# Optimization experiments

Hardware: AMD Instinct MI355X
Metric: run time of the kernel (lower is better)

## Reference

```python
import jax, jax.numpy as jnp
import numpy as np

SCALE = 8.0  # sqrt(d_k=64)


def setup_inputs() -> dict:
    key = jax.random.key(0)
    kq, kk, kv, km = jax.random.split(key, 4)
    B, L, D = 8, 4096, 64
    q = jax.random.normal(kq, (B, L, D), dtype=jnp.float32)
    k = jax.random.normal(kk, (B, L, D), dtype=jnp.float32)
    v = jax.random.normal(kv, (B, L, D), dtype=jnp.float32)
    mask = jax.random.randint(km, (B, L, L), 0, 2) == 1  # True = masked out
    return {"q": q, "k": k, "v": v, "mask": mask}


def reference(q, k, v, mask):
    # scores: [B, Lq, Lk]
    u = jnp.einsum('bqd,bkd->bqk', q, k) / SCALE
    u = jnp.where(mask, -jnp.inf, u)
    attn = jax.nn.softmax(u, axis=2)
    output = jnp.einsum('bqk,bkd->bqd', attn, v)
    return (attn, output)
```

## Files before the change

### kernel.cpp

```cpp
#include <hip/hip_runtime.h>
#include <hip/hip_bf16.h>
#include <stdint.h>

#define BB 8
#define LL 4096
#define DD 64
#define KT 64
#define NT (LL / KT)

typedef short bf16x8 __attribute__((ext_vector_type(8)));
typedef short bf16x4 __attribute__((ext_vector_type(4)));
typedef float f32x4 __attribute__((ext_vector_type(4)));

#define QSCALE 0.1803368801111204f
#define PP 68
#define MP 72

__device__ inline short f2bfs(float x) {
    __hip_bfloat16 h = __float2bfloat16(x);
    return __builtin_bit_cast(short, h);
}

__device__ inline int swzK(int r) { return (r & 3) | (((r >> 3) & 1) << 2); }
__device__ inline int swzV(int r) { return (r & 7) ^ ((r >> 3) & 7); }

__device__ inline void wg_barrier() {
    asm volatile("s_waitcnt lgkmcnt(0)" ::: "memory");
    __builtin_amdgcn_s_barrier();
    __builtin_amdgcn_sched_barrier(0);
}

__global__ void detect_mask_kernel(const uint32_t* __restrict__ w, uint32_t* __restrict__ flag) {
    __shared__ int nonbin;
    if (threadIdx.x == 0) nonbin = 0;
    __syncthreads();
    int bad = 0;
    for (int i = threadIdx.x; i < 4096; i += 256) bad |= (w[i] > 1u) ? 1 : 0;
    if (bad) atomicOr(&nonbin, 1);
    __syncthreads();
    if (threadIdx.x == 0) *flag = (uint32_t)(nonbin != 0);
}

__global__ __launch_bounds__(512, 4) void fused_attn_kernel(
    const float* __restrict__ qg, const float* __restrict__ kg,
    const float* __restrict__ vg, const void* __restrict__ maskv,
    const uint32_t* __restrict__ flagp,
    float* __restrict__ attn, float* __restrict__ outp)
{
    __shared__ alignas(16) ushort Kt[2][KT * 64];
    __shared__ alignas(16) ushort Vt[2][64 * KT];
    __shared__ alignas(16) float  Pout[64 * PP];
    __shared__ alignas(16) uint8_t Mt[2][64 * MP];
    __shared__ float Rs[128];

    const int tid = (int)threadIdx.x;
    const int w   = tid >> 6, l = tid & 63;
    const int lr  = l & 15, lg = l >> 4;
    const int rg  = w & 3, ch = w >> 2;
    const int id  = (int)blockIdx.x;
    const int b   = id & 7;
    const int q0  = (id >> 3) * 64;
    const bool mbyte = (*flagp != 0);

    const float* kb = kg + (size_t)b * LL * DD;
    const float* vb = vg + (size_t)b * LL * DD;
    const uint8_t* mb8 = (const uint8_t*)maskv + (size_t)b * LL * LL;
    float* attnb = attn + (size_t)b * LL * LL;
    const int qrow = q0 + 16 * rg + lr;
    const int* mrow32 = (const int*)maskv + (size_t)b * LL * LL + (size_t)qrow * LL + ch * 32 + lg * 8;

    bf16x8 qf0, qf1;
    {
        const float* qp = qg + (size_t)(b * LL + qrow) * DD + lg * 8;
        f32x4 a0 = *(const f32x4*)(qp)      * QSCALE, a1 = *(const f32x4*)(qp + 4)  * QSCALE;
        f32x4 a2 = *(const f32x4*)(qp + 32) * QSCALE, a3 = *(const f32x4*)(qp + 36) * QSCALE;
        #pragma unroll
        for (int e = 0; e < 4; ++e) { qf0[e] = f2bfs(a0[e]); qf0[4 + e] = f2bfs(a1[e]); }
        #pragma unroll
        for (int e = 0; e < 4; ++e) { qf1[e] = f2bfs(a2[e]); qf1[4 + e] = f2bfs(a3[e]); }
    }

    const int sr = tid >> 4, sc = tid & 15;
    const int mr = tid >> 3, mc = tid & 7;
    f32x4 kS0, kS1, vS0, vS1;
    uint64_t mS = 0;

    auto issK = [&](int kt) {
        const float* p = kb + (size_t)(kt * KT + sr) * DD + sc * 4;
        kS0 = *(const f32x4*)p;
        kS1 = *(const f32x4*)(p + 32 * DD);
    };
    auto issV = [&](int kt) {
        const float* p = vb + (size_t)(kt * KT + sr) * DD + sc * 4;
        vS0 = *(const f32x4*)p;
        vS1 = *(const f32x4*)(p + 32 * DD);
    };
    auto issM = [&](int kt) {
        if (mbyte) mS = *(const uint64_t*)(mb8 + (size_t)(q0 + mr) * LL + kt * KT + mc * 8);
    };
    auto comK = [&](int buf) {
        bf16x4 a, c;
        #pragma unroll
        for (int e = 0; e < 4; ++e) { a[e] = f2bfs(kS0[e]); c[e] = f2bfs(kS1[e]); }
        *(bf16x4*)&Kt[buf][sr * 64 + (((sc >> 1) ^ swzK(sr)) << 3) + (sc & 1) * 4] = a;
        const int r1 = sr + 32;
        *(bf16x4*)&Kt[buf][r1 * 64 + (((sc >> 1) ^ swzK(r1)) << 3) + (sc & 1) * 4] = c;
    };
    auto comV = [&](int buf) {
        #pragma unroll
        for (int e = 0; e < 4; ++e) {
            const int d = sc * 4 + e;
            Vt[buf][d * 64 + (((sr >> 3) ^ swzV(d)) << 3) + (sr & 7)]        = (ushort)f2bfs(vS0[e]);
            Vt[buf][d * 64 + ((((sr + 32) >> 3) ^ swzV(d)) << 3) + (sr & 7)] = (ushort)f2bfs(vS1[e]);
        }
    };
    auto comM = [&](int buf) {
        if (mbyte) *(uint64_t*)&Mt[buf][mr * MP + mc * 8] = mS;
    };

    float rsum = 0.f;
    f32x4 oacc[4];
    #pragma unroll
    for (int g = 0; g < 4; ++g) { f32x4 z = {0.f, 0.f, 0.f, 0.f}; oacc[g] = z; }

    auto body1 = [&](int cur, int kt) {
        uint64_t mu = 0;
        int4 mi0 = {0,0,0,0}, mi1 = {0,0,0,0};
        if (mbyte) mu = *(const uint64_t*)&Mt[cur][(16 * rg + lr) * MP + ch * 32 + lg * 8];
        else { mi0 = *(const int4*)(mrow32 + kt * KT); mi1 = *(const int4*)(mrow32 + kt * KT + 4); }
        float p8[8];
        #pragma unroll
        for (int n = 0; n < 2; ++n) {
            const int krow = ch * 32 + ((lr >> 2) << 3) + (n << 2) + (lr & 3);
            bf16x8 k0 = *(const bf16x8*)&Kt[cur][krow * 64 + ((lg       ^ swzK(krow)) << 3)];
            bf16x8 k1 = *(const bf16x8*)&Kt[cur][krow * 64 + (((4 + lg) ^ swzK(krow)) << 3)];
            f32x4 c = {0.f, 0.f, 0.f, 0.f};
            c = __builtin_amdgcn_mfma_f32_16x16x32_bf16(k0, qf0, c, 0, 0, 0);
            c = __builtin_amdgcn_mfma_f32_16x16x32_bf16(k1, qf1, c, 0, 0, 0);
            #pragma unroll
            for (int j = 0; j < 4; ++j) {
                const int t = n * 4 + j;
                int mk;
                if (mbyte) mk = (int)((mu >> (8 * t)) & 0xffu);
                else {
                    const int4 mi = n ? mi1 : mi0;
                    mk = (j == 0) ? mi.x : (j == 1) ? mi.y : (j == 2) ? mi.z : mi.w;
                }
                const float pv = mk ? 0.f : exp2f(c[j]);
                rsum += pv;
                p8[t] = pv;
            }
        }
        bf16x8 pa;
        #pragma unroll
        for (int t = 0; t < 8; ++t) pa[t] = f2bfs(p8[t]);
        __builtin_amdgcn_s_setprio(1);
        #pragma unroll
        for (int g = 0; g < 4; ++g) {
            const int d = g * 16 + lr;
            bf16x8 vf = *(const bf16x8*)&Vt[cur][d * 64 + (((ch * 4 + lg) ^ swzV(d)) << 3)];
            oacc[g] = __builtin_amdgcn_mfma_f32_16x16x32_bf16(pa, vf, oacc[g], 0, 0, 0);
        }
        __builtin_amdgcn_s_setprio(0);
    };

    issK(0); issV(0); issM(0);
    comK(0); comV(0); comM(0);
    wg_barrier();
    #pragma unroll 1
    for (int kt = 0; kt < NT; ++kt) {
        const int cur = kt & 1;
        const bool more = (kt < NT - 1);
        if (more) { issK(kt + 1); issV(kt + 1); issM(kt + 1); }
        body1(cur, kt);
        if (more) { comK(cur ^ 1); comV(cur ^ 1); comM(cur ^ 1); }
        wg_barrier();
    }

    rsum += __shfl_xor(rsum, 16, 64);
    rsum += __shfl_xor(rsum, 32, 64);
    if (lg == 0) Rs[ch * 64 + 16 * rg + lr] = rsum;
    __syncthreads();
    const float rinv = 1.0f / (Rs[16 * rg + lr] + Rs[64 + 16 * rg + lr]);

    issK(0); issM(0);

    if (ch == 1) {
        #pragma unroll
        for (int g = 0; g < 4; ++g)
            #pragma unroll
            for (int j = 0; j < 4; ++j)
                Pout[(16 * rg + lg * 4 + j) * PP + g * 16 + lr] = oacc[g][j];
    }
    __syncthreads();
    if (ch == 0) {
        #pragma unroll
        for (int j = 0; j < 4; ++j) {
            const int ql = 16 * rg + lg * 4 + j;
            const float ri = 1.0f / (Rs[ql] + Rs[64 + ql]);
            const size_t orow = (size_t)(b * LL + q0 + ql) * DD;
            #pragma unroll
            for (int g = 0; g < 4; ++g)
                outp[orow + g * 16 + lr] = (oacc[g][j] + Pout[ql * PP + g * 16 + lr]) * ri;
        }
    }
    comK(0); comM(0);
    wg_barrier();

    const int rr = tid >> 3, cc = tid & 7;
    auto body2 = [&](int cur, int kt) {
        uint64_t mu = 0;
        int4 mi0 = {0,0,0,0}, mi1 = {0,0,0,0};
        if (mbyte) mu = *(const uint64_t*)&Mt[cur][(16 * rg + lr) * MP + ch * 32 + lg * 8];
        else { mi0 = *(const int4*)(mrow32 + kt * KT); mi1 = *(const int4*)(mrow32 + kt * KT + 4); }
        #pragma unroll
        for (int n = 0; n < 2; ++n) {
            const int krow = ch * 32 + ((lr >> 2) << 3) + (n << 2) + (lr & 3);
            bf16x8 k0 = *(const bf16x8*)&Kt[cur][krow * 64 + ((lg       ^ swzK(krow)) << 3)];
            bf16x8 k1 = *(const bf16x8*)&Kt[cur][krow * 64 + (((4 + lg) ^ swzK(krow)) << 3)];
            f32x4 c = {0.f, 0.f, 0.f, 0.f};
            c = __builtin_amdgcn_mfma_f32_16x16x32_bf16(k0, qf0, c, 0, 0, 0);
            c = __builtin_amdgcn_mfma_f32_16x16x32_bf16(k1, qf1, c, 0, 0, 0);
            f32x4 pv;
            #pragma unroll
            for (int j = 0; j < 4; ++j) {
                const int t = n * 4 + j;
                int mk;
                if (mbyte) mk = (int)((mu >> (8 * t)) & 0xffu);
                else {
                    const int4 mi = n ? mi1 : mi0;
                    mk = (j == 0) ? mi.x : (j == 1) ? mi.y : (j == 2) ? mi.z : mi.w;
                }
                pv[j] = mk ? 0.f : exp2f(c[j]) * rinv;
            }
            *(f32x4*)&Pout[(16 * rg + lr) * PP + ch * 32 + lg * 8 + n * 4] = pv;
        }
    };

    #pragma unroll 1
    for (int kt = 0; kt < NT; ++kt) {
        const int cur = kt & 1;
        const bool more = (kt < NT - 1);
        if (more) { issK(kt + 1); issM(kt + 1); }
        body2(cur, kt);
        wg_barrier();
        {
            float4 v0 = *(const float4*)&Pout[rr * PP + cc * 4];
            float4 v1 = *(const float4*)&Pout[rr * PP + 32 + cc * 4];
            float* dst = attnb + (size_t)(q0 + rr) * LL + kt * KT + cc * 4;
            *(float4*)dst = v0;
            *(float4*)(dst + 32) = v1;
        }
        if (more) { comK(cur ^ 1); comM(cur ^ 1); }
        wg_barrier();
    }
}

extern "C" void kernel_launch(void* const* d_in, const int* in_sizes, int n_in,
                              void* d_out, int out_size, void* d_ws, size_t ws_size,
                              hipStream_t stream) {
    const float* q = (const float*)d_in[0];
    const float* k = (const float*)d_in[1];
    const float* v = (const float*)d_in[2];
    const void* mask = d_in[3];
    float* attn = (float*)d_out;
    float* outp = attn + (size_t)BB * LL * LL;
    uint32_t* flagp = (uint32_t*)d_ws;

    detect_mask_kernel<<<1, 256, 0, stream>>>((const uint32_t*)mask, flagp);
    fused_attn_kernel<<<dim3((LL / 64) * BB), 512, 0, stream>>>(q, k, v, mask, flagp, attn, outp);
}
```

Measured before the change: 427.8 us.

## Halve query block to 32 rows, write attn directly from registers

The query tile per workgroup drops from 64 rows with 512 threads to 32 rows with 256 threads, doubling the grid, and each thread now loads four K/V rows per tile instead of two. The second pass writes normalized attention probabilities straight to global memory from registers, dropping the shared-memory Pout staging buffer and one barrier per tile. The output reduction reuses the K tile buffer, and the setprio hints are removed. The risks are more K/V re-reads from global memory across the larger grid and less-coalesced 16-byte stores per lane for the attention matrix.

```diff
diff --git a/kernel.cpp b/kernel.cpp
--- a/kernel.cpp
+++ b/kernel.cpp
@@ -7,14 +7,15 @@
 #define DD 64
 #define KT 64
 #define NT (LL / KT)
+#define QBLK 32
+#define MP 72
 
 typedef short bf16x8 __attribute__((ext_vector_type(8)));
 typedef short bf16x4 __attribute__((ext_vector_type(4)));
+typedef short bf16x2 __attribute__((ext_vector_type(2)));
 typedef float f32x4 __attribute__((ext_vector_type(4)));
 
 #define QSCALE 0.1803368801111204f
-#define PP 68
-#define MP 72
 
 __device__ inline short f2bfs(float x) {
     __hip_bfloat16 h = __float2bfloat16(x);
@@ -41,7 +42,7 @@
     if (threadIdx.x == 0) *flag = (uint32_t)(nonbin != 0);
 }
 
-__global__ __launch_bounds__(512, 4) void fused_attn_kernel(
+__global__ __launch_bounds__(256, 4) void fused_attn_kernel(
     const float* __restrict__ qg, const float* __restrict__ kg,
     const float* __restrict__ vg, const void* __restrict__ maskv,
     const uint32_t* __restrict__ flagp,
@@ -49,25 +50,24 @@
 {
     __shared__ alignas(16) ushort Kt[2][KT * 64];
     __shared__ alignas(16) ushort Vt[2][64 * KT];
-    __shared__ alignas(16) float  Pout[64 * PP];
-    __shared__ alignas(16) uint8_t Mt[2][64 * MP];
-    __shared__ float Rs[128];
+    __shared__ alignas(16) uint8_t Mt[2][QBLK * MP];
+    __shared__ float Rs[2][QBLK];
 
     const int tid = (int)threadIdx.x;
     const int w   = tid >> 6, l = tid & 63;
     const int lr  = l & 15, lg = l >> 4;
-    const int rg  = w & 3, ch = w >> 2;
+    const int rg  = w & 1, ch = w >> 1;
     const int id  = (int)blockIdx.x;
     const int b   = id & 7;
-    const int q0  = (id >> 3) * 64;
+    const int q0  = (id >> 3) * QBLK;
     const bool mbyte = (*flagp != 0);
 
     const float* kb = kg + (size_t)b * LL * DD;
     const float* vb = vg + (size_t)b * LL * DD;
     const uint8_t* mb8 = (const uint8_t*)maskv + (size_t)b * LL * LL;
-    float* attnb = attn + (size_t)b * LL * LL;
     const int qrow = q0 + 16 * rg + lr;
     const int* mrow32 = (const int*)maskv + (size_t)b * LL * LL + (size_t)qrow * LL + ch * 32 + lg * 8;
+    float* arow = attn + (size_t)b * LL * LL + (size_t)qrow * LL + ch * 32 + lg * 8;
 
     bf16x8 qf0, qf1;
     {
@@ -82,36 +82,46 @@
 
     const int sr = tid >> 4, sc = tid & 15;
     const int mr = tid >> 3, mc = tid & 7;
-    f32x4 kS0, kS1, vS0, vS1;
+    f32x4 kS[4], vS[4];
     uint64_t mS = 0;
 
     auto issK = [&](int kt) {
-        const float* p = kb + (size_t)(kt * KT + sr) * DD + sc * 4;
-        kS0 = *(const f32x4*)p;
-        kS1 = *(const f32x4*)(p + 32 * DD);
+        #pragma unroll
+        for (int it = 0; it < 4; ++it)
+            kS[it] = *(const f32x4*)(kb + (size_t)(kt * KT + sr + 16 * it) * DD + sc * 4);
     };
     auto issV = [&](int kt) {
-        const float* p = vb + (size_t)(kt * KT + sr) * DD + sc * 4;
-        vS0 = *(const f32x4*)p;
-        vS1 = *(const f32x4*)(p + 32 * DD);
+        #pragma unroll
+        for (int it = 0; it < 4; ++it) {
+            const int r = 2 * sr + (it & 1) + 32 * (it >> 1);
+            vS[it] = *(const f32x4*)(vb + (size_t)(kt * KT + r) * DD + sc * 4);
+        }
     };
     auto issM = [&](int kt) {
         if (mbyte) mS = *(const uint64_t*)(mb8 + (size_t)(q0 + mr) * LL + kt * KT + mc * 8);
     };
     auto comK = [&](int buf) {
-        bf16x4 a, c;
-        #pragma unroll
-        for (int e = 0; e < 4; ++e) { a[e] = f2bfs(kS0[e]); c[e] = f2bfs(kS1[e]); }
-        *(bf16x4*)&Kt[buf][sr * 64 + (((sc >> 1) ^ swzK(sr)) << 3) + (sc & 1) * 4] = a;
-        const int r1 = sr + 32;
-        *(bf16x4*)&Kt[buf][r1 * 64 + (((sc >> 1) ^ swzK(r1)) << 3) + (sc & 1) * 4] = c;
+        #pragma unroll
+        for (int it = 0; it < 4; ++it) {
+            const int row = sr + 16 * it;
+            bf16x4 t;
+            #pragma unroll
+            for (int e = 0; e < 4; ++e) t[e] = f2bfs(kS[it][e]);
+            *(bf16x4*)&Kt[buf][row * 64 + (((sc >> 1) ^ swzK(row)) << 3) + (sc & 1) * 4] = t;
+        }
     };
     auto comV = [&](int buf) {
         #pragma unroll
-        for (int e = 0; e < 4; ++e) {
-            const int d = sc * 4 + e;
-            Vt[buf][d * 64 + (((sr >> 3) ^ swzV(d)) << 3) + (sr & 7)]        = (ushort)f2bfs(vS0[e]);
-            Vt[buf][d * 64 + ((((sr + 32) >> 3) ^ swzV(d)) << 3) + (sr & 7)] = (ushort)f2bfs(vS1[e]);
+        for (int p = 0; p < 2; ++p) {
+            const int k0 = 2 * sr + 32 * p;
+            #pragma unroll
+            for (int e = 0; e < 4; ++e) {
+                const int d = sc * 4 + e;
+                bf16x2 t;
+                t[0] = f2bfs(vS[2 * p][e]);
+                t[1] = f2bfs(vS[2 * p + 1][e]);
+                *(bf16x2*)&Vt[buf][d * 64 + (((k0 >> 3) ^ swzV(d)) << 3) + (k0 & 7)] = t;
+            }
         }
     };
     auto comM = [&](int buf) {
@@ -154,14 +164,12 @@
         bf16x8 pa;
         #pragma unroll
         for (int t = 0; t < 8; ++t) pa[t] = f2bfs(p8[t]);
-        __builtin_amdgcn_s_setprio(1);
         #pragma unroll
         for (int g = 0; g < 4; ++g) {
             const int d = g * 16 + lr;
             bf16x8 vf = *(const bf16x8*)&Vt[cur][d * 64 + (((ch * 4 + lg) ^ swzV(d)) << 3)];
             oacc[g] = __builtin_amdgcn_mfma_f32_16x16x32_bf16(pa, vf, oacc[g], 0, 0, 0);
         }
-        __builtin_amdgcn_s_setprio(0);
     };
 
     issK(0); issV(0); issM(0);
@@ -179,35 +187,32 @@
 
     rsum += __shfl_xor(rsum, 16, 64);
     rsum += __shfl_xor(rsum, 32, 64);
-    if (lg == 0) Rs[ch * 64 + 16 * rg + lr] = rsum;
-    __syncthreads();
-    const float rinv = 1.0f / (Rs[16 * rg + lr] + Rs[64 + 16 * rg + lr]);
-
-    issK(0); issM(0);
-
+    if (lg == 0) Rs[ch][16 * rg + lr] = rsum;
+    __syncthreads();
+    const float rinv = 1.0f / (Rs[0][16 * rg + lr] + Rs[1][16 * rg + lr]);
+
+    float* OutL = (float*)Kt;
     if (ch == 1) {
         #pragma unroll
         for (int g = 0; g < 4; ++g)
             #pragma unroll
             for (int j = 0; j < 4; ++j)
-                Pout[(16 * rg + lg * 4 + j) * PP + g * 16 + lr] = oacc[g][j];
+                OutL[(16 * rg + lg * 4 + j) * 68 + g * 16 + lr] = oacc[g][j];
     }
     __syncthreads();
     if (ch == 0) {
         #pragma unroll
         for (int j = 0; j < 4; ++j) {
             const int ql = 16 * rg + lg * 4 + j;
-            const float ri = 1.0f / (Rs[ql] + Rs[64 + ql]);
+            const float ri = 1.0f / (Rs[0][ql] + Rs[1][ql]);
             const size_t orow = (size_t)(b * LL + q0 + ql) * DD;
             #pragma unroll
             for (int g = 0; g < 4; ++g)
-                outp[orow + g * 16 + lr] = (oacc[g][j] + Pout[ql * PP + g * 16 + lr]) * ri;
-        }
-    }
-    comK(0); comM(0);
-    wg_barrier();
-
-    const int rr = tid >> 3, cc = tid & 7;
+                outp[orow + g * 16 + lr] = (oacc[g][j] + OutL[ql * 68 + g * 16 + lr]) * ri;
+        }
+    }
+    __syncthreads();
+
     auto body2 = [&](int cur, int kt) {
         uint64_t mu = 0;
         int4 mi0 = {0,0,0,0}, mi1 = {0,0,0,0};
@@ -233,24 +238,19 @@
                 }
                 pv[j] = mk ? 0.f : exp2f(c[j]) * rinv;
             }
-            *(f32x4*)&Pout[(16 * rg + lr) * PP + ch * 32 + lg * 8 + n * 4] = pv;
-        }
-    };
-
+            *(f32x4*)(arow + kt * KT + n * 4) = pv;
+        }
+    };
+
+    issK(0); issM(0);
+    comK(0); comM(0);
+    wg_barrier();
     #pragma unroll 1
     for (int kt = 0; kt < NT; ++kt) {
         const int cur = kt & 1;
         const bool more = (kt < NT - 1);
         if (more) { issK(kt + 1); issM(kt + 1); }
         body2(cur, kt);
-        wg_barrier();
-        {
-            float4 v0 = *(const float4*)&Pout[rr * PP + cc * 4];
-            float4 v1 = *(const float4*)&Pout[rr * PP + 32 + cc * 4];
-            float* dst = attnb + (size_t)(q0 + rr) * LL + kt * KT + cc * 4;
-            *(float4*)dst = v0;
-            *(float4*)(dst + 32) = v1;
-        }
         if (more) { comK(cur ^ 1); comM(cur ^ 1); }
         wg_barrier();
     }
@@ -268,5 +268,5 @@
     uint32_t* flagp = (uint32_t*)d_ws;
 
     detect_mask_kernel<<<1, 256, 0, stream>>>((const uint32_t*)mask, flagp);
-    fused_attn_kernel<<<dim3((LL / 64) * BB), 512, 0, stream>>>(q, k, v, mask, flagp, attn, outp);
-}
+    fused_attn_kernel<<<dim3((LL / QBLK) * BB), 256, 0, stream>>>(q, k, v, mask, flagp, attn, outp);
+}
```

New measurement: 487.1 us. 13.9% more time.
